# Optimization experiments

Hardware: AMD Instinct MI355X
Metric: run time of the kernel (lower is better)

Reference implementation:

```python
import jax, jax.numpy as jnp
import numpy as np

N = 100000
E = 1600000
FEAT = 128
EMB = 64
HID = 64
OUT = 16


def _glorot(key, shape):
    fan_in, fan_out = shape[1], shape[0]
    lim = (6.0 / (fan_in + fan_out)) ** 0.5
    return jax.random.uniform(key, shape, jnp.float32, -lim, lim)


def setup_inputs() -> dict:
    key = jax.random.key(0)
    ks = jax.random.split(key, 16)
    return {
        "x_feat": jax.random.normal(ks[0], (N, FEAT), jnp.float32),
        "x_emb": jax.random.normal(ks[1], (N, 2, EMB), jnp.float32),
        "edge_index": jax.random.randint(ks[2], (2, E), 0, N, jnp.int32),
        # layer 0: SAGEConv(FEAT -> HID), Linear(EMB -> HID)
        "Wl0": _glorot(ks[3], (HID, FEAT)),
        "bl0": jnp.zeros((HID,), jnp.float32),
        "Wr0": _glorot(ks[4], (HID, FEAT)),
        "We0": _glorot(ks[5], (HID, EMB)),
        "be0": jnp.zeros((HID,), jnp.float32),
        # layer 1 (last): SAGEConv(HID -> OUT), Linear(EMB==HID -> OUT)
        "Wl1": _glorot(ks[6], (OUT, HID)),
        "bl1": jnp.zeros((OUT,), jnp.float32),
        "Wr1": _glorot(ks[7], (OUT, HID)),
        "We1": _glorot(ks[8], (OUT, HID)),
        "be1": jnp.zeros((OUT,), jnp.float32),
    }


def _sage_conv(x, edge_index, Wl, bl, Wr):
    # PyG SAGEConv with mean aggregation:
    #   out = lin_l(mean_{j in N(i)} x_j) + lin_r(x_i)
    src, dst = edge_index[0], edge_index[1]
    msg = x[src]                                   # [E, C] gather
    agg = jax.ops.segment_sum(msg, dst, num_segments=N)       # [N, C]
    deg = jax.ops.segment_sum(jnp.ones((E,), x.dtype), dst, num_segments=N)
    agg = agg / jnp.maximum(deg, 1.0)[:, None]     # mean over neighbors
    return agg @ Wl.T + bl + x @ Wr.T


def reference(x_feat, x_emb, edge_index,
              Wl0, bl0, Wr0, We0, be0,
              Wl1, bl1, Wr1, We1, be1):
    # forward(x=(x_feat, x_emb), edge_index=...) path, eval mode (dropout p=0)
    e = x_emb.mean(axis=1)                         # [N, EMB]
    # layer 0 (all but last): relu(sage + linear(emb))
    h = _sage_conv(x_feat, edge_index, Wl0, bl0, Wr0)
    e = e @ We0.T + be0
    h = jax.nn.relu(h + e)
    # last layer: no relu
    h = _sage_conv(h, edge_index, Wl1, bl1, Wr1)
    e = e @ We1.T + be1
    return h + e
```

## Files before the change

### kernel.cpp

```cpp
#include <hip/hip_runtime.h>
#include <hip/hip_bf16.h>
#include <cstddef>

#define NN 100000
#define EE 1600000
#define NPB 128
#define NB  782
#define ECH 4096
#define NCH 391
#define CAP 6144

typedef __attribute__((ext_vector_type(8))) short bf16x8;
typedef __attribute__((ext_vector_type(4))) float f32x4;

static inline int ceil_div(int a, int b){ return (a + b - 1) / b; }

__device__ inline unsigned short f2bf(float f){
  union { float f; unsigned u; } v; v.f = f;
  unsigned r = (v.u + 0x7fff + ((v.u >> 16) & 1)) >> 16;
  return (unsigned short)r;
}
__device__ inline float bf2f(unsigned short s){
  union { unsigned u; float f; } v; v.u = ((unsigned)s) << 16;
  return v.f;
}

__global__ void prep_we_kernel(const float* __restrict__ We1, const float* __restrict__ We0,
                               const float* __restrict__ be0, const float* __restrict__ be1,
                               float* __restrict__ wee, float* __restrict__ b1e){
  int idx = blockIdx.x * blockDim.x + threadIdx.x;
  if (idx < 16 * 64){
    int i = idx >> 6, j = idx & 63;
    float s = 0.f;
    for (int k = 0; k < 64; k++) s += We1[i * 64 + k] * We0[k * 64 + j];
    wee[idx] = s;
  } else if (idx < 16 * 64 + 16){
    int i = idx - 16 * 64;
    float s = be1[i];
    for (int k = 0; k < 64; k++) s += We1[i * 64 + k] * be0[k];
    b1e[i] = s;
  }
}

__global__ void prep_wcat_kernel(const float* __restrict__ Wl0, const float* __restrict__ Wr0,
                                 const float* __restrict__ We0,
                                 unsigned short* __restrict__ wcat){
  int idx = blockIdx.x * blockDim.x + threadIdx.x;
  if (idx >= 128 * 192) return;
  int n = idx / 192, k = idx % 192;
  float v;
  if (n < 64) v = (k < 128) ? Wl0[n * 128 + k] : 0.f;
  else        v = (k < 128) ? Wr0[(n - 64) * 128 + k] : We0[(n - 64) * 64 + (k - 128)];
  wcat[idx] = f2bf(v);
}

__global__ __launch_bounds__(256) void escatter_kernel(const int* __restrict__ src,
                                                       const int* __restrict__ dst,
                                                       int* __restrict__ cur,
                                                       int* __restrict__ ebkt){
  __shared__ int lh[NB];
  __shared__ int lo[NB];
  int t = threadIdx.x;
  int e0 = blockIdx.x * ECH;
  int ne = EE - e0; if (ne > ECH) ne = ECH;
  for (int i = t; i < NB; i += 256) lh[i] = 0;
  __syncthreads();
  for (int i = t; i < ne; i += 256)
    atomicAdd(&lh[dst[e0 + i] >> 7], 1);
  __syncthreads();
  for (int i = t; i < NB; i += 256){
    int c = lh[i];
    lo[i] = c ? atomicAdd(&cur[i], c) : 0;
    lh[i] = 0;
  }
  __syncthreads();
  for (int i = t; i < ne; i += 256){
    int d = dst[e0 + i], b = d >> 7;
    int r = atomicAdd(&lh[b], 1);
    int p = lo[b] + r;
    if (p < CAP) ebkt[b * CAP + p] = ((d & 127) << 24) | src[e0 + i];
  }
}

__global__ __launch_bounds__(256) void bsort_kernel(
    const int* __restrict__ cur, int* __restrict__ ebkt,
    int* __restrict__ rs, int* __restrict__ deg){
  __shared__ int lraw[CAP];
  __shared__ int lout[CAP];
  __shared__ int lh[NPB];
  __shared__ int loff[NPB];
  __shared__ int lcur[NPB];
  const int t = threadIdx.x;
  const int b = blockIdx.x;
  const int e0 = b * CAP;
  int cnt = cur[b];
  if (cnt > CAP) cnt = CAP;
  for (int i = t; i < NPB; i += 256) lh[i] = 0;
  __syncthreads();
  for (int i = t; i < cnt; i += 256){
    int w = ebkt[e0 + i];
    lraw[i] = w;
    atomicAdd(&lh[((unsigned)w) >> 24], 1);
  }
  __syncthreads();
  {
    int v = (t < NPB) ? lh[t] : 0;
    int s = v;
    for (int off = 1; off < NPB; off <<= 1){
      int x = 0;
      if (t < NPB && t >= off) x = loff[t - off];
      __syncthreads();
      if (t < NPB) loff[t] = s;
      __syncthreads();
      if (t < NPB && t >= off) s += loff[t - off];
      __syncthreads();
    }
    if (t < NPB){ loff[t] = s - v; lcur[t] = s - v; }
  }
  __syncthreads();
  for (int i = t; i < cnt; i += 256){
    int w = lraw[i];
    int d = ((unsigned)w) >> 24;
    int pos = atomicAdd(&lcur[d], 1);
    lout[pos] = w & 0xFFFFFF;
  }
  __syncthreads();
  for (int i = t; i < cnt; i += 256) ebkt[e0 + i] = lout[i];
  if (t < NPB){
    int node = b * NPB + t;
    if (node < NN){
      rs[node]  = e0 + loff[t];
      deg[node] = lh[t];
    }
  }
}

__global__ __launch_bounds__(256, 4) void l0_gemm_kernel(
    const float* __restrict__ x_feat, const float* __restrict__ x_emb,
    const unsigned short* __restrict__ wcat,
    unsigned short* __restrict__ y0, float* __restrict__ re0,
    unsigned short* __restrict__ e_bf, int M){
  __shared__ unsigned short As[64 * 200];
  const int t = threadIdx.x;
  const int row0 = blockIdx.x * 64;
  float4 tmpa[12], tmpb[12];
  int rr[12], qq[12];
  #pragma unroll
  for (int k = 0; k < 12; k++){
    int idx = t + k * 256;
    int r = idx / 48, q = idx % 48;
    rr[k] = r; qq[k] = q;
    int row = row0 + r;
    float4 v = make_float4(0.f, 0.f, 0.f, 0.f);
    float4 u = make_float4(0.f, 0.f, 0.f, 0.f);
    if (row < M){
      if (q < 32){
        v = ((const float4*)x_feat)[(size_t)row * 32 + q];
      } else {
        v = ((const float4*)x_emb)[(size_t)row * 32 + (q - 32)];
        u = ((const float4*)x_emb)[(size_t)row * 32 + 16 + (q - 32)];
      }
    }
    tmpa[k] = v; tmpb[k] = u;
  }
  #pragma unroll
  for (int k = 0; k < 12; k++){
    int r = rr[k], q = qq[k];
    int row = row0 + r;
    float4 v = tmpa[k];
    if (q >= 32){
      float4 u = tmpb[k];
      v.x = 0.5f * (v.x + u.x); v.y = 0.5f * (v.y + u.y);
      v.z = 0.5f * (v.z + u.z); v.w = 0.5f * (v.w + u.w);
    }
    ushort4 s; s.x = f2bf(v.x); s.y = f2bf(v.y); s.z = f2bf(v.z); s.w = f2bf(v.w);
    *(ushort4*)&As[r * 200 + q * 4] = s;
    if (q >= 32 && row < M)
      *(ushort4*)&e_bf[(size_t)row * 64 + (q - 32) * 4] = s;
  }
  const int w = t >> 6, l = t & 63;
  const int lm = l & 15, quad = l >> 4;
  bf16x8 bfr0[6], bfr1[6];
  {
    int n0 = w * 16 + lm;
    int n1 = 64 + w * 16 + lm;
    #pragma unroll
    for (int ks = 0; ks < 6; ks++){
      bfr0[ks] = *(const bf16x8*)&wcat[n0 * 192 + ks * 32 + quad * 8];
      bfr1[ks] = *(const bf16x8*)&wcat[n1 * 192 + ks * 32 + quad * 8];
    }
  }
  __syncthreads();
  for (int rg = 0; rg < 4; rg++){
    bf16x8 af[6];
    #pragma unroll
    for (int ks = 0; ks < 6; ks++)
      af[ks] = *(const bf16x8*)&As[(rg * 16 + lm) * 200 + ks * 32 + quad * 8];
    f32x4 acc0 = {0.f, 0.f, 0.f, 0.f};
    f32x4 acc1 = {0.f, 0.f, 0.f, 0.f};
    #pragma unroll
    for (int ks = 0; ks < 6; ks++){
      acc0 = __builtin_amdgcn_mfma_f32_16x16x32_bf16(af[ks], bfr0[ks], acc0, 0, 0, 0);
      acc1 = __builtin_amdgcn_mfma_f32_16x16x32_bf16(af[ks], bfr1[ks], acc1, 0, 0, 0);
    }
    #pragma unroll
    for (int r = 0; r < 4; r++){
      int grow = row0 + rg * 16 + quad * 4 + r;
      if (grow < M){
        y0[(size_t)grow * 64 + w * 16 + lm]  = f2bf(acc0[r]);
        re0[(size_t)grow * 64 + w * 16 + lm] = acc1[r];
      }
    }
  }
}

__global__ void agg0_kernel(const unsigned short* __restrict__ y0,
                            const float4* __restrict__ re0,
                            const float* __restrict__ bl0, const float* __restrict__ be0,
                            const int* __restrict__ rs, const int* __restrict__ deg,
                            const int* __restrict__ ssrc, float4* __restrict__ h){
  int g = blockIdx.x * blockDim.x + threadIdx.x;
  if (g >= NN * 16) return;
  int node = g >> 4, lane = g & 15;
  int start = rs[node], cnt = deg[node];
  float acc[4][4] = {};
  int i = 0;
  for (; i + 8 <= cnt; i += 8){
    int s[8];
    #pragma unroll
    for (int j = 0; j < 8; j++) s[j] = ssrc[start + i + j];
    ushort4 v[8];
    #pragma unroll
    for (int j = 0; j < 8; j++) v[j] = *(const ushort4*)&y0[(size_t)s[j] * 64 + lane * 4];
    #pragma unroll
    for (int j = 0; j < 8; j++){
      acc[j & 3][0] += bf2f(v[j].x); acc[j & 3][1] += bf2f(v[j].y);
      acc[j & 3][2] += bf2f(v[j].z); acc[j & 3][3] += bf2f(v[j].w);
    }
  }
  for (; i + 4 <= cnt; i += 4){
    int s[4];
    #pragma unroll
    for (int j = 0; j < 4; j++) s[j] = ssrc[start + i + j];
    #pragma unroll
    for (int j = 0; j < 4; j++){
      ushort4 v = *(const ushort4*)&y0[(size_t)s[j] * 64 + lane * 4];
      acc[j][0] += bf2f(v.x); acc[j][1] += bf2f(v.y);
      acc[j][2] += bf2f(v.z); acc[j][3] += bf2f(v.w);
    }
  }
  for (; i < cnt; i++){
    int s = ssrc[start + i];
    ushort4 v = *(const ushort4*)&y0[(size_t)s * 64 + lane * 4];
    acc[0][0] += bf2f(v.x); acc[0][1] += bf2f(v.y); acc[0][2] += bf2f(v.z); acc[0][3] += bf2f(v.w);
  }
  float sx = (acc[0][0] + acc[1][0]) + (acc[2][0] + acc[3][0]);
  float sy = (acc[0][1] + acc[1][1]) + (acc[2][1] + acc[3][1]);
  float sz = (acc[0][2] + acc[1][2]) + (acc[2][2] + acc[3][2]);
  float sw = (acc[0][3] + acc[1][3]) + (acc[2][3] + acc[3][3]);
  float inv = 1.0f / (float)(cnt > 1 ? cnt : 1);
  float4 rv = re0[(size_t)node * 16 + lane];
  float4 b1 = ((const float4*)bl0)[lane];
  float4 b2 = ((const float4*)be0)[lane];
  float4 v;
  v.x = sx * inv + rv.x + b1.x + b2.x;
  v.y = sy * inv + rv.y + b1.y + b2.y;
  v.z = sz * inv + rv.z + b1.z + b2.z;
  v.w = sw * inv + rv.w + b1.w + b2.w;
  v.x = v.x > 0.f ? v.x : 0.f;
  v.y = v.y > 0.f ? v.y : 0.f;
  v.z = v.z > 0.f ? v.z : 0.f;
  v.w = v.w > 0.f ? v.w : 0.f;
  h[(size_t)node * 16 + lane] = v;
}

__global__ __launch_bounds__(256) void gemm16_dual_kernel(
    const float* __restrict__ H, const unsigned short* __restrict__ E,
    const float* __restrict__ Wl1, const float* __restrict__ Wr1,
    const float* __restrict__ wee,
    const float* __restrict__ bl1, const float* __restrict__ b1e,
    unsigned short* __restrict__ Y1, float* __restrict__ Out, int M){
  __shared__ float Hs[64][65];
  __shared__ float Es[64][65];
  __shared__ float Wls[16][65];
  __shared__ float Wrs[16][65];
  __shared__ float Wes[16][65];
  __shared__ float bs[16];
  const int t = threadIdx.x;
  const int row0 = blockIdx.x * 64;
  {
    int j = t >> 4, kq = t & 15;
    float4 a = ((const float4*)Wl1)[j * 16 + kq];
    float4 b = ((const float4*)Wr1)[j * 16 + kq];
    float4 c = ((const float4*)wee)[j * 16 + kq];
    Wls[j][kq*4+0]=a.x; Wls[j][kq*4+1]=a.y; Wls[j][kq*4+2]=a.z; Wls[j][kq*4+3]=a.w;
    Wrs[j][kq*4+0]=b.x; Wrs[j][kq*4+1]=b.y; Wrs[j][kq*4+2]=b.z; Wrs[j][kq*4+3]=b.w;
    Wes[j][kq*4+0]=c.x; Wes[j][kq*4+1]=c.y; Wes[j][kq*4+2]=c.z; Wes[j][kq*4+3]=c.w;
  }
  if (t < 16) bs[t] = bl1[t] + b1e[t];
  for (int idx = t; idx < 64 * 16; idx += 256){
    int n = idx >> 4, kq = idx & 15;
    int row = row0 + n;
    float4 v = make_float4(0.f,0.f,0.f,0.f);
    ushort4 u = make_ushort4(0, 0, 0, 0);
    if (row < M){
      v = ((const float4*)H)[(size_t)row * 16 + kq];
      u = *(const ushort4*)&E[(size_t)row * 64 + kq * 4];
    }
    Hs[n][kq*4+0]=v.x; Hs[n][kq*4+1]=v.y; Hs[n][kq*4+2]=v.z; Hs[n][kq*4+3]=v.w;
    Es[n][kq*4+0]=bf2f(u.x); Es[n][kq*4+1]=bf2f(u.y); Es[n][kq*4+2]=bf2f(u.z); Es[n][kq*4+3]=bf2f(u.w);
  }
  __syncthreads();
  const int n = t >> 2, jq = t & 3;
  float y[4] = {}, o[4] = {};
  #pragma unroll 4
  for (int k = 0; k < 64; k++){
    float a = Hs[n][k];
    float e = Es[n][k];
    #pragma unroll
    for (int j = 0; j < 4; j++){
      y[j] = fmaf(a, Wls[jq*4 + j][k], y[j]);
      o[j] = fmaf(a, Wrs[jq*4 + j][k], o[j]);
      o[j] = fmaf(e, Wes[jq*4 + j][k], o[j]);
    }
  }
  int row = row0 + n;
  if (row < M){
    ushort4 yb; yb.x = f2bf(y[0]); yb.y = f2bf(y[1]); yb.z = f2bf(y[2]); yb.w = f2bf(y[3]);
    *(ushort4*)&Y1[(size_t)row * 16 + jq * 4] = yb;
    ((float4*)Out)[(size_t)row * 4 + jq] =
        make_float4(o[0] + bs[jq*4+0], o[1] + bs[jq*4+1], o[2] + bs[jq*4+2], o[3] + bs[jq*4+3]);
  }
}

__global__ void agg1_kernel(const unsigned short* __restrict__ y1,
                            const int* __restrict__ rs, const int* __restrict__ deg,
                            const int* __restrict__ ssrc, float4* __restrict__ outp){
  int g = blockIdx.x * blockDim.x + threadIdx.x;
  if (g >= NN * 4) return;
  int node = g >> 2, lane = g & 3;
  int start = rs[node], cnt = deg[node];
  float acc[4][4] = {};
  int i = 0;
  for (; i + 8 <= cnt; i += 8){
    int s[8];
    #pragma unroll
    for (int j = 0; j < 8; j++) s[j] = ssrc[start + i + j];
    ushort4 v[8];
    #pragma unroll
    for (int j = 0; j < 8; j++) v[j] = *(const ushort4*)&y1[(size_t)s[j] * 16 + lane * 4];
    #pragma unroll
    for (int j = 0; j < 8; j++){
      acc[j & 3][0] += bf2f(v[j].x); acc[j & 3][1] += bf2f(v[j].y);
      acc[j & 3][2] += bf2f(v[j].z); acc[j & 3][3] += bf2f(v[j].w);
    }
  }
  for (; i + 4 <= cnt; i += 4){
    int s[4];
    #pragma unroll
    for (int j = 0; j < 4; j++) s[j] = ssrc[start + i + j];
    #pragma unroll
    for (int j = 0; j < 4; j++){
      ushort4 v = *(const ushort4*)&y1[(size_t)s[j] * 16 + lane * 4];
      acc[j][0] += bf2f(v.x); acc[j][1] += bf2f(v.y);
      acc[j][2] += bf2f(v.z); acc[j][3] += bf2f(v.w);
    }
  }
  for (; i < cnt; i++){
    int s = ssrc[start + i];
    ushort4 v = *(const ushort4*)&y1[(size_t)s * 16 + lane * 4];
    acc[0][0] += bf2f(v.x); acc[0][1] += bf2f(v.y); acc[0][2] += bf2f(v.z); acc[0][3] += bf2f(v.w);
  }
  float sx = (acc[0][0] + acc[1][0]) + (acc[2][0] + acc[3][0]);
  float sy = (acc[0][1] + acc[1][1]) + (acc[2][1] + acc[3][1]);
  float sz = (acc[0][2] + acc[1][2]) + (acc[2][2] + acc[3][2]);
  float sw = (acc[0][3] + acc[1][3]) + (acc[2][3] + acc[3][3]);
  float inv = 1.0f / (float)(cnt > 1 ? cnt : 1);
  float4 o = outp[(size_t)node * 4 + lane];
  o.x += sx * inv;
  o.y += sy * inv;
  o.z += sz * inv;
  o.w += sw * inv;
  outp[(size_t)node * 4 + lane] = o;
}

extern "C" void kernel_launch(void* const* d_in, const int* in_sizes, int n_in,
                              void* d_out, int out_size, void* d_ws, size_t ws_size,
                              hipStream_t stream){
  (void)in_sizes; (void)n_in; (void)out_size; (void)ws_size;
  const float* x_feat = (const float*)d_in[0];
  const float* x_emb  = (const float*)d_in[1];
  const int*   ei     = (const int*)d_in[2];
  const float* Wl0 = (const float*)d_in[3];
  const float* bl0 = (const float*)d_in[4];
  const float* Wr0 = (const float*)d_in[5];
  const float* We0 = (const float*)d_in[6];
  const float* be0 = (const float*)d_in[7];
  const float* Wl1 = (const float*)d_in[8];
  const float* bl1 = (const float*)d_in[9];
  const float* Wr1 = (const float*)d_in[10];
  const float* We1 = (const float*)d_in[11];
  const float* be1 = (const float*)d_in[12];
  float* out = (float*)d_out;

  char* w = (char*)d_ws;
  float* re0   = (float*)w;                  w += sizeof(float) * (size_t)NN * 64;
  float* h     = (float*)w;                  w += sizeof(float) * (size_t)NN * 64;
  unsigned short* y0  = (unsigned short*)w;  w += sizeof(unsigned short) * (size_t)NN * 64;
  unsigned short* e_bf= (unsigned short*)w;  w += sizeof(unsigned short) * (size_t)NN * 64;
  unsigned short* y1  = (unsigned short*)w;  w += sizeof(unsigned short) * (size_t)NN * 16;
  unsigned short* wcat= (unsigned short*)w;  w += sizeof(unsigned short) * 128 * 192;
  float* wee   = (float*)w;                  w += sizeof(float) * 16 * 64;
  float* b1e   = (float*)w;                  w += sizeof(float) * 16;
  int* ebkt    = (int*)w;                    w += sizeof(int) * (size_t)NB * CAP;
  int* cur     = (int*)w;                    w += sizeof(int) * NB;
  int* rs      = (int*)w;                    w += sizeof(int) * NN;
  int* deg     = (int*)w;                    w += sizeof(int) * NN;

  const int* srcp = ei;
  const int* dstp = ei + EE;

  hipMemsetAsync(cur, 0, sizeof(int) * NB, stream);

  prep_we_kernel<<<5, 256, 0, stream>>>(We1, We0, be0, be1, wee, b1e);
  prep_wcat_kernel<<<ceil_div(128 * 192, 256), 256, 0, stream>>>(Wl0, Wr0, We0, wcat);

  escatter_kernel<<<NCH, 256, 0, stream>>>(srcp, dstp, cur, ebkt);
  bsort_kernel<<<NB, 256, 0, stream>>>(cur, ebkt, rs, deg);

  l0_gemm_kernel<<<ceil_div(NN, 64), 256, 0, stream>>>(x_feat, x_emb, wcat, y0, re0, e_bf, NN);

  agg0_kernel<<<ceil_div(NN * 16, 256), 256, 0, stream>>>(
      y0, (const float4*)re0, bl0, be0, rs, deg, ebkt, (float4*)h);

  gemm16_dual_kernel<<<ceil_div(NN, 64), 256, 0, stream>>>(h, e_bf, Wl1, Wr1, wee,
                                                           bl1, b1e, y1, out, NN);
  agg1_kernel<<<ceil_div(NN * 4, 256), 256, 0, stream>>>(y1, rs, deg, ebkt, (float4*)out);
}
```

Measured before the change: 336.0 us.

## Stage GEMM outputs through LDS, store hidden state as bf16, merge prep kernels

The layer-0 GEMM now writes its y0 and re0 results into shared memory first and then stores them to global memory as wide vector writes, replacing the strided scalar stores. The intermediate hidden activation h is now stored in bf16 instead of fp32, which halves its write traffic in agg0 and its read traffic in the second GEMM, at some cost in precision. The two weight-prep kernels are merged into one launch, and bias0 = bl0 + be0 is precomputed there. The GEMM occupancy hint drops from 4 to 3 blocks because of the extra shared memory.

```diff
diff --git a/kernel.cpp b/kernel.cpp
--- a/kernel.cpp
+++ b/kernel.cpp
@@ -11,7 +11,11 @@
 #define CAP 6144
 
 typedef __attribute__((ext_vector_type(8))) short bf16x8;
+typedef __attribute__((ext_vector_type(8))) unsigned short u16x8;
 typedef __attribute__((ext_vector_type(4))) float f32x4;
+
+#define Y0S 72
+#define RES 68
 
 static inline int ceil_div(int a, int b){ return (a + b - 1) / b; }
 
@@ -25,33 +29,34 @@
   return v.f;
 }
 
-__global__ void prep_we_kernel(const float* __restrict__ We1, const float* __restrict__ We0,
-                               const float* __restrict__ be0, const float* __restrict__ be1,
-                               float* __restrict__ wee, float* __restrict__ b1e){
+__global__ void prep_all_kernel(const float* __restrict__ Wl0, const float* __restrict__ Wr0,
+                                const float* __restrict__ We0, const float* __restrict__ bl0,
+                                const float* __restrict__ be0, const float* __restrict__ We1,
+                                const float* __restrict__ be1,
+                                unsigned short* __restrict__ wcat, float* __restrict__ wee,
+                                float* __restrict__ b1e, float* __restrict__ bias0){
   int idx = blockIdx.x * blockDim.x + threadIdx.x;
-  if (idx < 16 * 64){
-    int i = idx >> 6, j = idx & 63;
+  if (idx < 128 * 192){
+    int n = idx / 192, k = idx % 192;
+    float v;
+    if (n < 64) v = (k < 128) ? Wl0[n * 128 + k] : 0.f;
+    else        v = (k < 128) ? Wr0[(n - 64) * 128 + k] : We0[(n - 64) * 64 + (k - 128)];
+    wcat[idx] = f2bf(v);
+  } else if (idx < 128 * 192 + 16 * 64){
+    int j = idx - 128 * 192;
+    int i = j >> 6, c = j & 63;
     float s = 0.f;
-    for (int k = 0; k < 64; k++) s += We1[i * 64 + k] * We0[k * 64 + j];
-    wee[idx] = s;
-  } else if (idx < 16 * 64 + 16){
-    int i = idx - 16 * 64;
+    for (int k = 0; k < 64; k++) s += We1[i * 64 + k] * We0[k * 64 + c];
+    wee[j] = s;
+  } else if (idx < 128 * 192 + 16 * 64 + 16){
+    int i = idx - (128 * 192 + 16 * 64);
     float s = be1[i];
     for (int k = 0; k < 64; k++) s += We1[i * 64 + k] * be0[k];
     b1e[i] = s;
-  }
-}
-
-__global__ void prep_wcat_kernel(const float* __restrict__ Wl0, const float* __restrict__ Wr0,
-                                 const float* __restrict__ We0,
-                                 unsigned short* __restrict__ wcat){
-  int idx = blockIdx.x * blockDim.x + threadIdx.x;
-  if (idx >= 128 * 192) return;
-  int n = idx / 192, k = idx % 192;
-  float v;
-  if (n < 64) v = (k < 128) ? Wl0[n * 128 + k] : 0.f;
-  else        v = (k < 128) ? Wr0[(n - 64) * 128 + k] : We0[(n - 64) * 64 + (k - 128)];
-  wcat[idx] = f2bf(v);
+  } else if (idx < 128 * 192 + 16 * 64 + 16 + 64){
+    int i = idx - (128 * 192 + 16 * 64 + 16);
+    bias0[i] = bl0[i] + be0[i];
+  }
 }
 
 __global__ __launch_bounds__(256) void escatter_kernel(const int* __restrict__ src,
@@ -135,28 +140,27 @@
   }
 }
 
-__global__ __launch_bounds__(256, 4) void l0_gemm_kernel(
+__global__ __launch_bounds__(256, 3) void l0_gemm_kernel(
     const float* __restrict__ x_feat, const float* __restrict__ x_emb,
     const unsigned short* __restrict__ wcat,
-    unsigned short* __restrict__ y0, float* __restrict__ re0,
+    unsigned short* __restrict__ y0g, float* __restrict__ re0g,
     unsigned short* __restrict__ e_bf, int M){
   __shared__ unsigned short As[64 * 200];
+  __shared__ unsigned short Ys[64 * Y0S];
+  __shared__ float          Rs[64 * RES];
   const int t = threadIdx.x;
   const int row0 = blockIdx.x * 64;
   float4 tmpa[12], tmpb[12];
-  int rr[12], qq[12];
   #pragma unroll
   for (int k = 0; k < 12; k++){
     int idx = t + k * 256;
     int r = idx / 48, q = idx % 48;
-    rr[k] = r; qq[k] = q;
     int row = row0 + r;
     float4 v = make_float4(0.f, 0.f, 0.f, 0.f);
     float4 u = make_float4(0.f, 0.f, 0.f, 0.f);
     if (row < M){
-      if (q < 32){
-        v = ((const float4*)x_feat)[(size_t)row * 32 + q];
-      } else {
+      if (q < 32) v = ((const float4*)x_feat)[(size_t)row * 32 + q];
+      else {
         v = ((const float4*)x_emb)[(size_t)row * 32 + (q - 32)];
         u = ((const float4*)x_emb)[(size_t)row * 32 + 16 + (q - 32)];
       }
@@ -165,7 +169,8 @@
   }
   #pragma unroll
   for (int k = 0; k < 12; k++){
-    int r = rr[k], q = qq[k];
+    int idx = t + k * 256;
+    int r = idx / 48, q = idx % 48;
     int row = row0 + r;
     float4 v = tmpa[k];
     if (q >= 32){
@@ -205,20 +210,39 @@
     }
     #pragma unroll
     for (int r = 0; r < 4; r++){
-      int grow = row0 + rg * 16 + quad * 4 + r;
-      if (grow < M){
-        y0[(size_t)grow * 64 + w * 16 + lm]  = f2bf(acc0[r]);
-        re0[(size_t)grow * 64 + w * 16 + lm] = acc1[r];
-      }
+      int lrow = rg * 16 + quad * 4 + r;
+      Ys[lrow * Y0S + w * 16 + lm] = f2bf(acc0[r]);
+      Rs[lrow * RES + w * 16 + lm] = acc1[r];
+    }
+  }
+  __syncthreads();
+  #pragma unroll
+  for (int k = 0; k < 2; k++){
+    int idx = t + k * 256;
+    int r = idx >> 3, c8 = idx & 7;
+    int grow = row0 + r;
+    if (grow < M){
+      u16x8 v = *(const u16x8*)&Ys[r * Y0S + c8 * 8];
+      *(u16x8*)&y0g[(size_t)grow * 64 + c8 * 8] = v;
+    }
+  }
+  #pragma unroll
+  for (int k = 0; k < 4; k++){
+    int idx = t + k * 256;
+    int r = idx >> 4, c4 = idx & 15;
+    int grow = row0 + r;
+    if (grow < M){
+      f32x4 v = *(const f32x4*)&Rs[r * RES + c4 * 4];
+      *(f32x4*)&re0g[(size_t)grow * 64 + c4 * 4] = v;
     }
   }
 }
 
 __global__ void agg0_kernel(const unsigned short* __restrict__ y0,
                             const float4* __restrict__ re0,
-                            const float* __restrict__ bl0, const float* __restrict__ be0,
+                            const float* __restrict__ bias0,
                             const int* __restrict__ rs, const int* __restrict__ deg,
-                            const int* __restrict__ ssrc, float4* __restrict__ h){
+                            const int* __restrict__ ssrc, unsigned short* __restrict__ h){
   int g = blockIdx.x * blockDim.x + threadIdx.x;
   if (g >= NN * 16) return;
   int node = g >> 4, lane = g & 15;
@@ -260,22 +284,21 @@
   float sw = (acc[0][3] + acc[1][3]) + (acc[2][3] + acc[3][3]);
   float inv = 1.0f / (float)(cnt > 1 ? cnt : 1);
   float4 rv = re0[(size_t)node * 16 + lane];
-  float4 b1 = ((const float4*)bl0)[lane];
-  float4 b2 = ((const float4*)be0)[lane];
-  float4 v;
-  v.x = sx * inv + rv.x + b1.x + b2.x;
-  v.y = sy * inv + rv.y + b1.y + b2.y;
-  v.z = sz * inv + rv.z + b1.z + b2.z;
-  v.w = sw * inv + rv.w + b1.w + b2.w;
-  v.x = v.x > 0.f ? v.x : 0.f;
-  v.y = v.y > 0.f ? v.y : 0.f;
-  v.z = v.z > 0.f ? v.z : 0.f;
-  v.w = v.w > 0.f ? v.w : 0.f;
-  h[(size_t)node * 16 + lane] = v;
+  float4 bb = ((const float4*)bias0)[lane];
+  float vx = sx * inv + rv.x + bb.x;
+  float vy = sy * inv + rv.y + bb.y;
+  float vz = sz * inv + rv.z + bb.z;
+  float vw = sw * inv + rv.w + bb.w;
+  vx = vx > 0.f ? vx : 0.f;
+  vy = vy > 0.f ? vy : 0.f;
+  vz = vz > 0.f ? vz : 0.f;
+  vw = vw > 0.f ? vw : 0.f;
+  ushort4 o; o.x = f2bf(vx); o.y = f2bf(vy); o.z = f2bf(vz); o.w = f2bf(vw);
+  *(ushort4*)&h[(size_t)node * 64 + lane * 4] = o;
 }
 
 __global__ __launch_bounds__(256) void gemm16_dual_kernel(
-    const float* __restrict__ H, const unsigned short* __restrict__ E,
+    const unsigned short* __restrict__ H, const unsigned short* __restrict__ E,
     const float* __restrict__ Wl1, const float* __restrict__ Wr1,
     const float* __restrict__ wee,
     const float* __restrict__ bl1, const float* __restrict__ b1e,
@@ -301,14 +324,13 @@
   for (int idx = t; idx < 64 * 16; idx += 256){
     int n = idx >> 4, kq = idx & 15;
     int row = row0 + n;
-    float4 v = make_float4(0.f,0.f,0.f,0.f);
-    ushort4 u = make_ushort4(0, 0, 0, 0);
+    ushort4 hv = make_ushort4(0,0,0,0), ev = make_ushort4(0,0,0,0);
     if (row < M){
-      v = ((const float4*)H)[(size_t)row * 16 + kq];
-      u = *(const ushort4*)&E[(size_t)row * 64 + kq * 4];
-    }
-    Hs[n][kq*4+0]=v.x; Hs[n][kq*4+1]=v.y; Hs[n][kq*4+2]=v.z; Hs[n][kq*4+3]=v.w;
-    Es[n][kq*4+0]=bf2f(u.x); Es[n][kq*4+1]=bf2f(u.y); Es[n][kq*4+2]=bf2f(u.z); Es[n][kq*4+3]=bf2f(u.w);
+      hv = *(const ushort4*)&H[(size_t)row * 64 + kq * 4];
+      ev = *(const ushort4*)&E[(size_t)row * 64 + kq * 4];
+    }
+    Hs[n][kq*4+0]=bf2f(hv.x); Hs[n][kq*4+1]=bf2f(hv.y); Hs[n][kq*4+2]=bf2f(hv.z); Hs[n][kq*4+3]=bf2f(hv.w);
+    Es[n][kq*4+0]=bf2f(ev.x); Es[n][kq*4+1]=bf2f(ev.y); Es[n][kq*4+2]=bf2f(ev.z); Es[n][kq*4+3]=bf2f(ev.w);
   }
   __syncthreads();
   const int n = t >> 2, jq = t & 3;
@@ -405,13 +427,14 @@
 
   char* w = (char*)d_ws;
   float* re0   = (float*)w;                  w += sizeof(float) * (size_t)NN * 64;
-  float* h     = (float*)w;                  w += sizeof(float) * (size_t)NN * 64;
+  unsigned short* h   = (unsigned short*)w;  w += sizeof(unsigned short) * (size_t)NN * 64;
   unsigned short* y0  = (unsigned short*)w;  w += sizeof(unsigned short) * (size_t)NN * 64;
   unsigned short* e_bf= (unsigned short*)w;  w += sizeof(unsigned short) * (size_t)NN * 64;
   unsigned short* y1  = (unsigned short*)w;  w += sizeof(unsigned short) * (size_t)NN * 16;
   unsigned short* wcat= (unsigned short*)w;  w += sizeof(unsigned short) * 128 * 192;
   float* wee   = (float*)w;                  w += sizeof(float) * 16 * 64;
   float* b1e   = (float*)w;                  w += sizeof(float) * 16;
+  float* bias0 = (float*)w;                  w += sizeof(float) * 64;
   int* ebkt    = (int*)w;                    w += sizeof(int) * (size_t)NB * CAP;
   int* cur     = (int*)w;                    w += sizeof(int) * NB;
   int* rs      = (int*)w;                    w += sizeof(int) * NN;
@@ -422,8 +445,8 @@
 
   hipMemsetAsync(cur, 0, sizeof(int) * NB, stream);
 
-  prep_we_kernel<<<5, 256, 0, stream>>>(We1, We0, be0, be1, wee, b1e);
-  prep_wcat_kernel<<<ceil_div(128 * 192, 256), 256, 0, stream>>>(Wl0, Wr0, We0, wcat);
+  prep_all_kernel<<<ceil_div(128*192 + 16*64 + 16 + 64, 256), 256, 0, stream>>>(
+      Wl0, Wr0, We0, bl0, be0, We1, be1, wcat, wee, b1e, bias0);
 
   escatter_kernel<<<NCH, 256, 0, stream>>>(srcp, dstp, cur, ebkt);
   bsort_kernel<<<NB, 256, 0, stream>>>(cur, ebkt, rs, deg);
@@ -431,7 +454,7 @@
   l0_gemm_kernel<<<ceil_div(NN, 64), 256, 0, stream>>>(x_feat, x_emb, wcat, y0, re0, e_bf, NN);
 
   agg0_kernel<<<ceil_div(NN * 16, 256), 256, 0, stream>>>(
-      y0, (const float4*)re0, bl0, be0, rs, deg, ebkt, (float4*)h);
+      y0, (const float4*)re0, bias0, rs, deg, ebkt, h);
 
   gemm16_dual_kernel<<<ceil_div(NN, 64), 256, 0, stream>>>(h, e_bf, Wl1, Wr1, wee,
                                                            bl1, b1e, y1, out, NN);
```

Result: faster. 315.9 us (-6.0%).
